# Optimization experiments

Measured on AMD Instinct MI355X. Metric: run time of the kernel, lower is better.

The kernel has to match this reference:

```python
import jax, jax.numpy as jnp
import numpy as np

D_MODEL = 1024
N_HEADS = 16
D_K = D_MODEL // N_HEADS
LORA_R = 8
SCALING = 16 / 8  # lora_alpha / lora_rank = 2.0


def setup_inputs() -> dict:
    key = jax.random.key(0)
    ks = jax.random.split(key, 12)
    s = 1.0 / np.sqrt(D_MODEL)
    inp = {
        "x": jax.random.normal(ks[0], (4, 2048, D_MODEL), dtype=jnp.float32),
        "w_q": jax.random.normal(ks[1], (D_MODEL, D_MODEL), dtype=jnp.float32) * s,
        "b_q": jnp.zeros((D_MODEL,), dtype=jnp.float32),
        "w_k": jax.random.normal(ks[2], (D_MODEL, D_MODEL), dtype=jnp.float32) * s,
        "b_k": jnp.zeros((D_MODEL,), dtype=jnp.float32),
        "w_v": jax.random.normal(ks[3], (D_MODEL, D_MODEL), dtype=jnp.float32) * s,
        "b_v": jnp.zeros((D_MODEL,), dtype=jnp.float32),
        "w_o": jax.random.normal(ks[4], (D_MODEL, D_MODEL), dtype=jnp.float32) * s,
        "b_o": jnp.zeros((D_MODEL,), dtype=jnp.float32),
        # LoRA: down [d_model -> r], up [r -> d_model]; up init nonzero here so grads flow
        "a_q": jax.random.normal(ks[5], (D_MODEL, LORA_R), dtype=jnp.float32) * s,
        "u_q": jax.random.normal(ks[6], (LORA_R, D_MODEL), dtype=jnp.float32) * 0.01,
        "a_k": jax.random.normal(ks[7], (D_MODEL, LORA_R), dtype=jnp.float32) * s,
        "u_k": jax.random.normal(ks[8], (LORA_R, D_MODEL), dtype=jnp.float32) * 0.01,
        "a_v": jax.random.normal(ks[9], (D_MODEL, LORA_R), dtype=jnp.float32) * s,
        "u_v": jax.random.normal(ks[10], (LORA_R, D_MODEL), dtype=jnp.float32) * 0.01,
    }
    return inp


def reference(x, w_q, b_q, w_k, b_k, w_v, b_v, w_o, b_o, a_q, u_q, a_k, u_k, a_v, u_v):
    B, S, D = x.shape
    # base projections + LoRA (eval mode: dropout off)
    q = x @ w_q + b_q + (x @ a_q) @ u_q * SCALING
    k = x @ w_k + b_k + (x @ a_k) @ u_k * SCALING
    v = x @ w_v + b_v + (x @ a_v) @ u_v * SCALING
    # [B, H, S, d_k]
    q = q.reshape(B, S, N_HEADS, D_K).transpose(0, 2, 1, 3)
    k = k.reshape(B, S, N_HEADS, D_K).transpose(0, 2, 1, 3)
    v = v.reshape(B, S, N_HEADS, D_K).transpose(0, 2, 1, 3)
    scores = jnp.einsum("bhsd,bhtd->bhst", q, k) / np.sqrt(D_K)
    probs = jax.nn.softmax(scores, axis=-1)
    out = jnp.einsum("bhst,bhtd->bhsd", probs, v)
    out = out.transpose(0, 2, 1, 3).reshape(B, S, D)
    return out @ w_o + b_o
```

## Files before the change

kernel.cpp:

```cpp
#include <hip/hip_runtime.h>
#include <stdint.h>

typedef unsigned short u16;
typedef unsigned int u32;
typedef __bf16 bf16x8 __attribute__((ext_vector_type(8)));
typedef __bf16 bf16x4 __attribute__((ext_vector_type(4)));
typedef float f32x4 __attribute__((ext_vector_type(4)));
typedef float f32x16 __attribute__((ext_vector_type(16)));
typedef u32 u32x4 __attribute__((ext_vector_type(4)));

#define SEQ 2048
#define QSCALE 0.1803368801111137f

__device__ __forceinline__ float fast_exp2(float x) { return __builtin_amdgcn_exp2f(x); }

__device__ __forceinline__ void async16(const void* g, void* l) {
  __builtin_amdgcn_global_load_lds((const __attribute__((address_space(1))) void*)g,
                                   (__attribute__((address_space(3))) void*)l, 16, 0, 0);
}

__device__ __forceinline__ u32 pkbf(float a, float b) {
  u16 xa = __builtin_bit_cast(u16, (__bf16)a);
  u16 xb = __builtin_bit_cast(u16, (__bf16)b);
  return (u32)xa | ((u32)xb << 16);
}


__global__ void prep_all_kernel(const float* __restrict__ x, u16* __restrict__ xb,
                                const float* __restrict__ wq, const float* __restrict__ wk,
                                const float* __restrict__ wv, const float* __restrict__ wo,
                                const float* __restrict__ aq, const float* __restrict__ ak,
                                const float* __restrict__ av,
                                const float* __restrict__ uq, const float* __restrict__ uk,
                                const float* __restrict__ uv,
                                u16* __restrict__ weffT,
                                const float* __restrict__ bq, const float* __restrict__ bk,
                                const float* __restrict__ bv, float* __restrict__ bias_qkv) {
  __shared__ float wt[32][33];
  __shared__ float at[32][8];
  __shared__ float ut[8][33];
  const int bid = blockIdx.x;
  const int t = threadIdx.x;
  if (bid < 8192) {
    int i = (bid * 256 + t) * 4;
    float4 v = *(const float4*)(x + i);
    bf16x4 o;
    o[0] = (__bf16)v.x; o[1] = (__bf16)v.y; o[2] = (__bf16)v.z; o[3] = (__bf16)v.w;
    *(bf16x4*)(xb + i) = o;
  } else if (bid < 12288) {
    const int p = (bid - 8192) >> 10, bx = (bid - 8192) & 1023;
    const int tn0 = (bx & 31) * 32, tk0 = (bx >> 5) * 32;
    const float* w = (p == 0) ? wq : (p == 1) ? wk : (p == 2) ? wv : wo;
    const float* a = (p == 0) ? aq : (p == 1) ? ak : av;
    const float* u = (p == 0) ? uq : (p == 1) ? uk : uv;
    {
      int tk = t >> 3, tn4 = (t & 7) * 4;
      float4 v = *(const float4*)(w + (tk0 + tk) * 1024 + tn0 + tn4);
      wt[tk][tn4] = v.x; wt[tk][tn4 + 1] = v.y; wt[tk][tn4 + 2] = v.z; wt[tk][tn4 + 3] = v.w;
    }
    if (p < 3) {
      at[t >> 3][t & 7] = a[(tk0 + (t >> 3)) * 8 + (t & 7)];
      ut[t >> 5][t & 31] = u[(t >> 5) * 1024 + tn0 + (t & 31)];
    }
    __syncthreads();
    const int tn = t >> 3, tk4 = (t & 7) * 4;
    bf16x4 o;
#pragma unroll
    for (int jj = 0; jj < 4; ++jj) {
      int k = tk4 + jj;
      float val = wt[k][tn];
      if (p < 3) {
        float acc = 0.f;
#pragma unroll
        for (int r = 0; r < 8; ++r) acc += at[k][r] * ut[r][tn];
        val += 2.0f * acc;
      }
      if (p == 0) val *= QSCALE;
      o[jj] = (__bf16)val;
    }
    *(bf16x4*)(weffT + p * 1048576 + (tn0 + tn) * 1024 + tk0 + tk4) = o;
  } else {
    int i = (bid - 12288) * 256 + t;
    bias_qkv[i] = (i < 1024) ? bq[i] * QSCALE : (i < 2048) ? bk[i - 1024] : bv[i - 2048];
  }
}


template <int MODE>
__global__ __launch_bounds__(256, 2)
void gemm_tt(const u16* __restrict__ U, const u16* __restrict__ V, void* __restrict__ OUT,
             u16* __restrict__ vT, const float* __restrict__ bias, const int NU, const int K) {
  __shared__ __align__(16) char smU[8192];
  __shared__ __align__(16) char smV[8192];
  const int t = threadIdx.x;
  const int lane = t & 63, ln = lane & 15, g = lane >> 4, w = t >> 6;
  const int u0 = blockIdx.x * 128, v0 = blockIdx.y * 128;
  const int wu = (w & 1) * 64, wv = (w >> 1) * 64;
  f32x4 acc[4][4] = {};
  for (int k0 = 0; k0 < K; k0 += 32) {
    __syncthreads();
#pragma unroll
    for (int half = 0; half < 2; ++half) {
      int p = half * 256 + t;
      int s = p >> 2, cp = p & 3;
      int c = cp ^ (s & 3);
      int ldsoff = (half * 256 + (t & 192)) * 16;
      async16(U + (u0 + s) * K + k0 + c * 8, smU + ldsoff);
      async16(V + (v0 + s) * K + k0 + c * 8, smV + ldsoff);
    }
    __syncthreads();
    bf16x8 af[4], bf[4];
#pragma unroll
    for (int mt = 0; mt < 4; ++mt)
      af[mt] = *(const bf16x8*)(smU + (wu + mt * 16 + ln) * 64 + ((g ^ (ln & 3)) * 16));
#pragma unroll
    for (int nt = 0; nt < 4; ++nt)
      bf[nt] = *(const bf16x8*)(smV + (wv + nt * 16 + ln) * 64 + ((g ^ (ln & 3)) * 16));
#pragma unroll
    for (int mt = 0; mt < 4; ++mt)
#pragma unroll
      for (int nt = 0; nt < 4; ++nt)
        acc[mt][nt] = __builtin_amdgcn_mfma_f32_16x16x32_bf16(af[mt], bf[nt], acc[mt][nt], 0, 0, 0);
  }
  const bool isV = (MODE == 1) && (u0 + wu >= 2048);
#pragma unroll
  for (int mt = 0; mt < 4; ++mt) {
    const int u = u0 + wu + mt * 16 + g * 4;
    const float4 bs = *(const float4*)(bias + u);
#pragma unroll
    for (int nt = 0; nt < 4; ++nt) {
      const int v = v0 + wv + nt * 16 + ln;
      f32x4 a = acc[mt][nt];
      a[0] += bs.x; a[1] += bs.y; a[2] += bs.z; a[3] += bs.w;
      if (MODE == 0) {
        *(float4*)((float*)OUT + (size_t)v * NU + u) = make_float4(a[0], a[1], a[2], a[3]);
      } else if (!isV) {
        bf16x4 o;
        o[0] = (__bf16)a[0]; o[1] = (__bf16)a[1]; o[2] = (__bf16)a[2]; o[3] = (__bf16)a[3];
        *(bf16x4*)((u16*)OUT + (size_t)v * 2048 + u) = o;
      } else {
        const int uu = u - 2048;
        const int hh = uu >> 6, dd = uu & 63;
        const int bb = v >> 11, ss = v & 2047;
        u16* dst = vT + ((size_t)((bb * 16 + hh) * 64 + dd)) * 2048 + ss;
#pragma unroll
        for (int r = 0; r < 4; ++r)
          *(__bf16*)(dst + (size_t)r * 2048) = (__bf16)a[r];
      }
    }
  }
}


__global__ __launch_bounds__(256, 3)
void attn_kernel(const u16* __restrict__ qkv, const u16* __restrict__ vT,
                 u16* __restrict__ attn_o) {
  __shared__ __align__(16) char smK[16384];
  __shared__ __align__(16) char smVt[16384];
  const int t = threadIdx.x;
  const int lane = t & 63, q32 = lane & 31, hf = lane >> 5, w = t >> 6;
  const int hd = blockIdx.x, qt = blockIdx.y, b = blockIdx.z;
  const int q0 = qt * 128;
  const size_t base_b = (size_t)b * SEQ * 2048;
  const u16* qbase = qkv + base_b + hd * 64;
  const u16* kbase0 = qkv + base_b + 1024 + hd * 64;
  const u16* vbase0 = vT + ((size_t)(b * 16 + hd) * 64) * 2048;

  bf16x8 qf[4];
#pragma unroll
  for (int ks = 0; ks < 4; ++ks)
    qf[ks] = *(const bf16x8*)(qbase + (size_t)(q0 + w * 32 + q32) * 2048 + ks * 16 + hf * 8);

  bf16x8 ones_frag;
  {
    u32 o2 = (q32 == 0) ? 0x3F803F80u : 0u;
    u32x4 ow = {o2, o2, o2, o2};
    ones_frag = __builtin_bit_cast(bf16x8, ow);
  }

  const u16* srcK[4];
  const u16* srcV[4];
  char* dstK[4];
  char* dstV[4];
#pragma unroll
  for (int i = 0; i < 4; ++i) {
    int p = i * 256 + t;
    {
      int row = p >> 3, cp = p & 7;
      int rowp = (row & ~12) | ((row & 4) << 1) | ((row & 8) >> 1);
      int c = cp ^ (row & 7);
      srcK[i] = kbase0 + (size_t)rowp * 2048 + c * 8;
      dstK[i] = smK + (i * 256 + (t & 192)) * 16;
    }
    {
      int d = p >> 4, cp = p & 15;
      int key = (d & 15) ^ (d >> 3);
      int c = (cp ^ key) & 15;
      srcV[i] = vbase0 + (size_t)d * 2048 + c * 8;
      dstV[i] = smVt + (i * 256 + (t & 192)) * 16;
    }
  }

  f32x16 accO[2] = {};
  f32x16 acc_l = {};

  for (int kt = 0; kt < 16; ++kt) {
    __syncthreads();
#pragma unroll
    for (int i = 0; i < 4; ++i) {
      async16(srcK[i], dstK[i]);
      srcK[i] += 128 * 2048;
    }
#pragma unroll
    for (int i = 0; i < 4; ++i) {
      async16(srcV[i], dstV[i]);
      srcV[i] += 128;
    }
    __syncthreads();

    f32x16 st[4] = {};
#pragma unroll
    for (int ks = 0; ks < 4; ++ks) {
#pragma unroll
      for (int c = 0; c < 4; ++c) {
        int row = c * 32 + q32;
        bf16x8 kfr = *(const bf16x8*)(smK + row * 128 + (((2 * ks + hf) ^ (row & 7)) * 16));
        st[c] = __builtin_amdgcn_mfma_f32_32x32x16_bf16(kfr, qf[ks], st[c], 0, 0, 0);
      }
    }

#pragma unroll
    for (int c = 0; c < 4; ++c) {
#pragma unroll
      for (int kh = 0; kh < 2; ++kh) {
        float e[8];
#pragma unroll
        for (int j = 0; j < 8; ++j) e[j] = fast_exp2(st[c][8 * kh + j]);
        u32x4 bw;
        bw[0] = pkbf(e[0], e[1]);
        bw[1] = pkbf(e[2], e[3]);
        bw[2] = pkbf(e[4], e[5]);
        bw[3] = pkbf(e[6], e[7]);
        bf16x8 pfrag = __builtin_bit_cast(bf16x8, bw);
        acc_l = __builtin_amdgcn_mfma_f32_32x32x16_bf16(ones_frag, pfrag, acc_l, 0, 0, 0);
#pragma unroll
        for (int mt = 0; mt < 2; ++mt) {
          int row = mt * 32 + q32;
          int key = (row & 15) ^ (row >> 3);
          bf16x8 vfr = *(const bf16x8*)(smVt + row * 256 +
                                        (((4 * c + 2 * kh + hf) ^ key) & 15) * 16);
          accO[mt] = __builtin_amdgcn_mfma_f32_32x32x16_bf16(vfr, pfrag, accO[mt], 0, 0, 0);
        }
      }
    }
  }

  float lv = __shfl(acc_l[0], q32);
  float il = 1.0f / lv;
  const int s = q0 + w * 32 + q32;
#pragma unroll
  for (int mt = 0; mt < 2; ++mt)
#pragma unroll
    for (int qd = 0; qd < 4; ++qd) {
      int d0 = 32 * mt + 8 * qd + 4 * hf;
      bf16x4 o;
#pragma unroll
      for (int r = 0; r < 4; ++r) o[r] = (__bf16)(accO[mt][4 * qd + r] * il);
      *(bf16x4*)(attn_o + (size_t)(b * SEQ + s) * 1024 + hd * 64 + d0) = o;
    }
}


extern "C" void kernel_launch(void* const* d_in, const int* in_sizes, int n_in,
                              void* d_out, int out_size, void* d_ws, size_t ws_size,
                              hipStream_t stream) {
  const float* x  = (const float*)d_in[0];
  const float* wq = (const float*)d_in[1];
  const float* bq = (const float*)d_in[2];
  const float* wk = (const float*)d_in[3];
  const float* bk = (const float*)d_in[4];
  const float* wv = (const float*)d_in[5];
  const float* bv = (const float*)d_in[6];
  const float* wo = (const float*)d_in[7];
  const float* bo = (const float*)d_in[8];
  const float* aq = (const float*)d_in[9];
  const float* uq = (const float*)d_in[10];
  const float* ak = (const float*)d_in[11];
  const float* uk = (const float*)d_in[12];
  const float* av = (const float*)d_in[13];
  const float* uv = (const float*)d_in[14];

  char* ws = (char*)d_ws;
  u16* xb       = (u16*)(ws);
  u16* attn_o   = (u16*)(ws);
  u16* qkv      = (u16*)(ws + (16u << 20));
  u16* vT       = (u16*)(ws + (48u << 20));
  u16* weffT    = (u16*)(ws + (64u << 20));
  float* biasq  = (float*)(ws + (72u << 20));

  prep_all_kernel<<<dim3(12300), dim3(256), 0, stream>>>(
      x, xb, wq, wk, wv, wo, aq, ak, av, uq, uk, uv, weffT, bq, bk, bv, biasq);
  gemm_tt<1><<<dim3(24, 64), dim3(256), 0, stream>>>(weffT, xb, (void*)qkv, vT, biasq, 2048, 1024);
  attn_kernel<<<dim3(16, 16, 4), dim3(256), 0, stream>>>(qkv, vT, attn_o);
  gemm_tt<0><<<dim3(8, 64), dim3(256), 0, stream>>>(weffT + 3u * 1048576u, attn_o, d_out, nullptr, bo, 1024, 1024);
}
```

Baseline: 314.6 us.

## Double-buffer K/V tiles and process two query subtiles per wave in attention

The attention kernel now prefetches the next K/V tile into a second LDS buffer while computing on the current one, which removes one barrier per iteration and overlaps loads with MFMA work. Each wave also handles 64 query rows (two 32-row subtiles), so every K and V fragment read from LDS feeds two MFMAs and the grid shrinks to half the blocks. The cost is doubled LDS and accumulator registers, with occupancy lowered to 2 blocks per SIMD set, and only 512 blocks remain to fill the GPU.

```diff
diff --git a/kernel.cpp b/kernel.cpp
--- a/kernel.cpp
+++ b/kernel.cpp
@@ -152,24 +152,27 @@
 }
 
 
-__global__ __launch_bounds__(256, 3)
+__global__ __launch_bounds__(256, 2)
 void attn_kernel(const u16* __restrict__ qkv, const u16* __restrict__ vT,
                  u16* __restrict__ attn_o) {
-  __shared__ __align__(16) char smK[16384];
-  __shared__ __align__(16) char smVt[16384];
+  __shared__ __align__(16) char smK[32768];
+  __shared__ __align__(16) char smVt[32768];
   const int t = threadIdx.x;
   const int lane = t & 63, q32 = lane & 31, hf = lane >> 5, w = t >> 6;
   const int hd = blockIdx.x, qt = blockIdx.y, b = blockIdx.z;
-  const int q0 = qt * 128;
+  const int q0 = qt * 256;
   const size_t base_b = (size_t)b * SEQ * 2048;
   const u16* qbase = qkv + base_b + hd * 64;
   const u16* kbase0 = qkv + base_b + 1024 + hd * 64;
   const u16* vbase0 = vT + ((size_t)(b * 16 + hd) * 64) * 2048;
 
-  bf16x8 qf[4];
+  bf16x8 qf[4][2];
 #pragma unroll
   for (int ks = 0; ks < 4; ++ks)
-    qf[ks] = *(const bf16x8*)(qbase + (size_t)(q0 + w * 32 + q32) * 2048 + ks * 16 + hf * 8);
+#pragma unroll
+    for (int nt = 0; nt < 2; ++nt)
+      qf[ks][nt] = *(const bf16x8*)(qbase + (size_t)(q0 + w * 64 + nt * 32 + q32) * 2048 +
+                                    ks * 16 + hf * 8);
 
   bf16x8 ones_frag;
   {
@@ -201,73 +204,94 @@
     }
   }
 
-  f32x16 accO[2] = {};
-  f32x16 acc_l = {};
+#pragma unroll
+  for (int i = 0; i < 4; ++i) {
+    async16(srcK[i], dstK[i]);
+    srcK[i] += 128 * 2048;
+  }
+#pragma unroll
+  for (int i = 0; i < 4; ++i) {
+    async16(srcV[i], dstV[i]);
+    srcV[i] += 128;
+  }
+  __syncthreads();
+
+  f32x16 accO[2][2] = {};
+  f32x16 acc_l[2] = {};
 
   for (int kt = 0; kt < 16; ++kt) {
-    __syncthreads();
-#pragma unroll
-    for (int i = 0; i < 4; ++i) {
-      async16(srcK[i], dstK[i]);
-      srcK[i] += 128 * 2048;
-    }
-#pragma unroll
-    for (int i = 0; i < 4; ++i) {
-      async16(srcV[i], dstV[i]);
-      srcV[i] += 128;
-    }
-    __syncthreads();
-
-    f32x16 st[4] = {};
-#pragma unroll
-    for (int ks = 0; ks < 4; ++ks) {
-#pragma unroll
-      for (int c = 0; c < 4; ++c) {
+    const int cur = kt & 1, nxt = cur ^ 1;
+    if (kt < 15) {
+#pragma unroll
+      for (int i = 0; i < 4; ++i) {
+        async16(srcK[i], dstK[i] + nxt * 16384);
+        srcK[i] += 128 * 2048;
+      }
+#pragma unroll
+      for (int i = 0; i < 4; ++i) {
+        async16(srcV[i], dstV[i] + nxt * 16384);
+        srcV[i] += 128;
+      }
+    }
+    const char* kbuf = smK + cur * 16384;
+    const char* vbuf = smVt + cur * 16384;
+
+#pragma unroll
+    for (int c = 0; c < 4; ++c) {
+      f32x16 stc[2] = {};
+#pragma unroll
+      for (int ks = 0; ks < 4; ++ks) {
         int row = c * 32 + q32;
-        bf16x8 kfr = *(const bf16x8*)(smK + row * 128 + (((2 * ks + hf) ^ (row & 7)) * 16));
-        st[c] = __builtin_amdgcn_mfma_f32_32x32x16_bf16(kfr, qf[ks], st[c], 0, 0, 0);
-      }
-    }
-
-#pragma unroll
-    for (int c = 0; c < 4; ++c) {
+        bf16x8 kfr = *(const bf16x8*)(kbuf + row * 128 + (((2 * ks + hf) ^ (row & 7)) * 16));
+        stc[0] = __builtin_amdgcn_mfma_f32_32x32x16_bf16(kfr, qf[ks][0], stc[0], 0, 0, 0);
+        stc[1] = __builtin_amdgcn_mfma_f32_32x32x16_bf16(kfr, qf[ks][1], stc[1], 0, 0, 0);
+      }
 #pragma unroll
       for (int kh = 0; kh < 2; ++kh) {
-        float e[8];
-#pragma unroll
-        for (int j = 0; j < 8; ++j) e[j] = fast_exp2(st[c][8 * kh + j]);
-        u32x4 bw;
-        bw[0] = pkbf(e[0], e[1]);
-        bw[1] = pkbf(e[2], e[3]);
-        bw[2] = pkbf(e[4], e[5]);
-        bw[3] = pkbf(e[6], e[7]);
-        bf16x8 pfrag = __builtin_bit_cast(bf16x8, bw);
-        acc_l = __builtin_amdgcn_mfma_f32_32x32x16_bf16(ones_frag, pfrag, acc_l, 0, 0, 0);
+        bf16x8 pfrag[2];
+#pragma unroll
+        for (int nt = 0; nt < 2; ++nt) {
+          float e[8];
+#pragma unroll
+          for (int j = 0; j < 8; ++j) e[j] = fast_exp2(stc[nt][8 * kh + j]);
+          u32x4 bw;
+          bw[0] = pkbf(e[0], e[1]);
+          bw[1] = pkbf(e[2], e[3]);
+          bw[2] = pkbf(e[4], e[5]);
+          bw[3] = pkbf(e[6], e[7]);
+          pfrag[nt] = __builtin_bit_cast(bf16x8, bw);
+          acc_l[nt] = __builtin_amdgcn_mfma_f32_32x32x16_bf16(ones_frag, pfrag[nt], acc_l[nt], 0, 0, 0);
+        }
 #pragma unroll
         for (int mt = 0; mt < 2; ++mt) {
           int row = mt * 32 + q32;
           int key = (row & 15) ^ (row >> 3);
-          bf16x8 vfr = *(const bf16x8*)(smVt + row * 256 +
+          bf16x8 vfr = *(const bf16x8*)(vbuf + row * 256 +
                                         (((4 * c + 2 * kh + hf) ^ key) & 15) * 16);
-          accO[mt] = __builtin_amdgcn_mfma_f32_32x32x16_bf16(vfr, pfrag, accO[mt], 0, 0, 0);
+          accO[mt][0] = __builtin_amdgcn_mfma_f32_32x32x16_bf16(vfr, pfrag[0], accO[mt][0], 0, 0, 0);
+          accO[mt][1] = __builtin_amdgcn_mfma_f32_32x32x16_bf16(vfr, pfrag[1], accO[mt][1], 0, 0, 0);
         }
       }
     }
-  }
-
-  float lv = __shfl(acc_l[0], q32);
-  float il = 1.0f / lv;
-  const int s = q0 + w * 32 + q32;
-#pragma unroll
-  for (int mt = 0; mt < 2; ++mt)
-#pragma unroll
-    for (int qd = 0; qd < 4; ++qd) {
-      int d0 = 32 * mt + 8 * qd + 4 * hf;
-      bf16x4 o;
-#pragma unroll
-      for (int r = 0; r < 4; ++r) o[r] = (__bf16)(accO[mt][4 * qd + r] * il);
-      *(bf16x4*)(attn_o + (size_t)(b * SEQ + s) * 1024 + hd * 64 + d0) = o;
-    }
+    if (kt < 15) __syncthreads();
+  }
+
+#pragma unroll
+  for (int nt = 0; nt < 2; ++nt) {
+    float lv = __shfl(acc_l[nt][0], q32);
+    float il = 1.0f / lv;
+    const int s = q0 + w * 64 + nt * 32 + q32;
+#pragma unroll
+    for (int mt = 0; mt < 2; ++mt)
+#pragma unroll
+      for (int qd = 0; qd < 4; ++qd) {
+        int d0 = 32 * mt + 8 * qd + 4 * hf;
+        bf16x4 o;
+#pragma unroll
+        for (int r = 0; r < 4; ++r) o[r] = (__bf16)(accO[mt][nt][4 * qd + r] * il);
+        *(bf16x4*)(attn_o + (size_t)(b * SEQ + s) * 1024 + hd * 64 + d0) = o;
+      }
+  }
 }
 
 
@@ -301,6 +325,6 @@
   prep_all_kernel<<<dim3(12300), dim3(256), 0, stream>>>(
       x, xb, wq, wk, wv, wo, aq, ak, av, uq, uk, uv, weffT, bq, bk, bv, biasq);
   gemm_tt<1><<<dim3(24, 64), dim3(256), 0, stream>>>(weffT, xb, (void*)qkv, vT, biasq, 2048, 1024);
-  attn_kernel<<<dim3(16, 16, 4), dim3(256), 0, stream>>>(qkv, vT, attn_o);
+  attn_kernel<<<dim3(16, 8, 4), dim3(256), 0, stream>>>(qkv, vT, attn_o);
   gemm_tt<0><<<dim3(8, 64), dim3(256), 0, stream>>>(weffT + 3u * 1048576u, attn_o, d_out, nullptr, bo, 1024, 1024);
 }
```

After: 298.0 us. 1.06x faster.
